# Performance work log

Hardware: AMD Instinct MI355X
Metric: run time of the kernel (lower is better)

## Reference

```python
import jax, jax.numpy as jnp
import numpy as np
from jax import lax

B, N, FIN, T, K, FC, FT = 8, 2048, 3, 12, 3, 64, 64


def _conv2d(x, w, b, pad):
    # x [B,C,N,T], w [O,I,1,kw], NCHW conv
    y = lax.conv_general_dilated(x, w, (1, 1), pad,
                                 dimension_numbers=('NCHW', 'OIHW', 'NCHW'))
    return y + b[None, :, None, None]


def _spatial_att(h, W, a, alpha, concat):
    # GAT-style dense attention. h [B,N,Fin], W [Fin,D], a [2D,1]
    D = W.shape[1]
    Wh = h @ W                                             # [B,N,D]
    e = jax.nn.leaky_relu(Wh @ a[:D] + jnp.swapaxes(Wh @ a[D:], 1, 2), alpha)  # [B,N,N]
    att = jax.nn.softmax(jax.nn.sigmoid(e), axis=1)        # softmax over dim=1 (as in torch)
    hp = jnp.einsum('bij,bjd->bid', att, Wh)
    return jax.nn.elu(hp) if concat else hp


def setup_inputs() -> dict:
    key = jax.random.key(0)
    ks = jax.random.split(key, 24)
    rnd = lambda i, shape, scale=1.0: (jax.random.normal(ks[i], shape, dtype=jnp.float32) * scale)
    FTm = FC * T  # 768 spatial-attention feature dim
    D = FTm // 2
    return {
        'x': rnd(0, (B, N, FIN, T)),
        'cheb': rnd(1, (K, N, N), 1.0 / np.sqrt(N)),
        'Gamma': rnd(2, (K, FIN, FC), 1.0 / np.sqrt(FIN)),
        'W_heads': rnd(3, (2, FTm, D), 1.0 / np.sqrt(FTm)),
        'a_heads': rnd(4, (2, 2 * D, 1), 1.0 / np.sqrt(2 * D)),
        'W_out': rnd(5, (FTm, FTm), 1.0 / np.sqrt(FTm)),
        'a_out': rnd(6, (2 * FTm, 1), 1.0 / np.sqrt(2 * FTm)),
        'U1': rnd(7, (FT, FT), 1.0 / np.sqrt(FT)),
        'U2': rnd(8, (FT,), 1.0 / np.sqrt(FT)),
        'U3': rnd(9, (FT,), 1.0 / np.sqrt(FT)),
        'be': rnd(10, (1, T, T), 0.1),
        'Ve': rnd(11, (T, T), 1.0 / np.sqrt(T)),
        'time_w': rnd(12, (FT, FC, 1, 3), 1.0 / np.sqrt(3 * FC)),
        'time_b': rnd(13, (FT,), 0.01),
        'res_w': rnd(14, (FT, FIN, 1, 1), 1.0 / np.sqrt(FIN)),
        'res_b': rnd(15, (FT,), 0.01),
        'back_w': rnd(16, (FT, FC, 1, 3), 1.0 / np.sqrt(3 * FC)),
        'back_b': rnd(17, (FT,), 0.01),
        'fore_w': rnd(18, (FT, FC, 1, 3), 1.0 / np.sqrt(3 * FC)),
        'fore_b': rnd(19, (FT,), 0.01),
        'ln_g': jnp.ones((FT,), jnp.float32),
        'ln_b': jnp.zeros((FT,), jnp.float32),
    }


def reference(x, cheb, Gamma, W_heads, a_heads, W_out, a_out, U1, U2, U3, be, Ve,
              time_w, time_b, res_w, res_b, back_w, back_b, fore_w, fore_b, ln_g, ln_b):
    b, n, fin, t = x.shape
    k_ = cheb.shape[0]
    fc = Gamma.shape[2]
    # ChebNetII interpolation coefficients T_k(x_j), x_j = cos((j+0.5)pi/K) -> [j,k]
    jj = np.arange(k_)
    cxj = jnp.asarray(np.cos(np.outer((jj + 0.5) * np.pi / k_, np.arange(k_))), x.dtype)
    lhs = jnp.einsum('jio,jk->kio', Gamma, cxj)                         # [K,Fin,Fc]
    rhs = jnp.einsum('bnit,knm->kbmit', x, cheb)                        # [K,B,N,Fin,T]
    spatial_gcn = jax.nn.relu((2.0 / (k_ + 1)) * jnp.einsum('kbmit,kio->bmot', rhs, lhs))  # [B,N,Fc,T]

    # Spatial transformer: 2 GAT heads + output attention
    h = spatial_gcn.reshape(b, n, fc * t)
    heads = jax.vmap(lambda W, a: _spatial_att(h, W, a, 0.1, True))(W_heads, a_heads)  # [H,B,N,D]
    hcat = jnp.transpose(heads, (1, 2, 0, 3)).reshape(b, n, -1)
    gcn_SAt = jax.nn.relu(_spatial_att(hcat, W_out, a_out, 0.1, False)).reshape(b, n, fc, t)

    # Temporal conv (1x3, pad 1)
    tc = _conv2d(jnp.transpose(gcn_SAt, (0, 2, 1, 3)), time_w, time_b, ((0, 0), (1, 1)))
    tc = jnp.transpose(tc, (0, 2, 1, 3))                                # [B,N,Ft,T]

    # Temporal attention
    lhs_t = jnp.einsum('bnft,fg,g->btn', tc, U1, U2)                    # [B,T,N]
    rhs_t = jnp.einsum('f,bnft->bnt', U3, tc)                           # [B,N,T]
    prod = jnp.einsum('bsn,bnt->bst', lhs_t, rhs_t)                     # [B,T,T]
    E = jnp.einsum('is,bst->bit', Ve, jax.nn.sigmoid(prod + be))
    E = jax.nn.softmax(E, axis=1)
    tcn = jnp.einsum('bnft,bts->bnfs', tc, E)                           # [B,N,Ft,T]

    # Residual (1x1 conv) + LayerNorm over channel dim
    x_res = _conv2d(jnp.transpose(x, (0, 2, 1, 3)), res_w, res_b, ((0, 0), (0, 0)))
    x_res = jnp.transpose(x_res, (0, 2, 1, 3))                          # [B,N,Ft,T]
    z = jnp.transpose(jax.nn.relu(x_res + tcn), (0, 3, 1, 2))           # [B,T,N,Ft]
    mu = z.mean(-1, keepdims=True)
    var = z.var(-1, keepdims=True)
    z = (z - mu) / jnp.sqrt(var + 1e-5) * ln_g + ln_b
    result = jnp.transpose(z, (0, 2, 3, 1))                             # [B,N,Ft,T]

    rp = jnp.transpose(result, (0, 2, 1, 3))
    backcast = jnp.transpose(_conv2d(rp, back_w, back_b, ((0, 0), (1, 1))), (0, 2, 1, 3))
    forecast = jnp.transpose(_conv2d(rp, fore_w, fore_b, ((0, 0), (1, 1))), (0, 2, 1, 3))
    return (backcast, forecast)
```

## Files before the change

### kernel.cpp

```cpp
#include <hip/hip_runtime.h>


typedef unsigned short u16;
typedef __bf16 bf16x8 __attribute__((ext_vector_type(8)));
typedef float f32x4 __attribute__((ext_vector_type(4)));
typedef u16 u16x8 __attribute__((ext_vector_type(8)));

__device__ __forceinline__ u16 f2b(float f) {
  union { float f; unsigned u; } v; v.f = f;
  unsigned u = v.u;
  u = u + 0x7FFFu + ((u >> 16) & 1u);
  return (u16)(u >> 16);
}
__device__ __forceinline__ float b2f(u16 h) {
  union { unsigned u; float f; } v; v.u = ((unsigned)h) << 16; return v.f;
}
__device__ __forceinline__ float qfun(float x) {
  float e = x > 0.f ? x : 0.1f * x;
  float s = __builtin_amdgcn_rcpf(1.f + __expf(-e));
  return __expf(s);
}

template <int N> __device__ __forceinline__ void waitvm() {
  if constexpr (N == 0)      asm volatile("s_waitcnt vmcnt(0)" ::: "memory");
  else if constexpr (N == 2) asm volatile("s_waitcnt vmcnt(2)" ::: "memory");
  else if constexpr (N == 4) asm volatile("s_waitcnt vmcnt(4)" ::: "memory");
  else if constexpr (N == 6) asm volatile("s_waitcnt vmcnt(6)" ::: "memory");
  else                       asm volatile("s_waitcnt vmcnt(8)" ::: "memory");
}
__device__ __forceinline__ void rawbar() { asm volatile("s_barrier" ::: "memory"); }

#define GLOAD16(g, l) __builtin_amdgcn_global_load_lds( \
    (__attribute__((address_space(1))) void*)(g),       \
    (__attribute__((address_space(3))) void*)(l), 16, 0, 0)

constexpr size_t OFF_LHS     = 0x0;
constexpr size_t OFF_U1U2    = 0x1000;
constexpr size_t OFF_BIASBIG = 0x1100;
constexpr size_t OFF_FH      = 0x3000;
constexpr size_t OFF_GH      = 0x23000;
constexpr size_t OFF_RDH     = 0x43000;
constexpr size_t OFF_FO      = 0x63000;
constexpr size_t OFF_GO      = 0x73000;
constexpr size_t OFF_RDO     = 0x83000;
constexpr size_t OFF_LHST    = 0x93000;
constexpr size_t OFF_RHST    = 0x153000;
constexpr size_t OFF_PROD    = 0x213000;
constexpr size_t OFF_E       = 0x215000;
constexpr size_t OFF_WCATT   = 0x220000;
constexpr size_t OFF_WOUTT   = 0x340000;
constexpr size_t OFF_WTBIG   = 0x460000;
constexpr size_t OFF_XCOLT   = 0x580000;
constexpr size_t OFF_CHEBT   = 0x700000;
constexpr size_t OFF_C1      = 0x1F00000;
constexpr size_t OFF_H       = 0x4300000;
constexpr size_t OFF_P       = 0x700000;
constexpr size_t OFF_WHCATT  = 0x5B00000;
constexpr size_t OFF_HCAT    = 0x7300000;
constexpr size_t OFF_WHOUTT  = 0x5B00000;
constexpr size_t OFF_GCNB    = 0x7300000;
constexpr size_t OFF_WBFBIG  = 0x8B00000;
constexpr size_t OFF_TCS     = 0x700000;
constexpr size_t OFF_RESULTB = 0x3700000;
constexpr size_t WS_NEEDED   = 0x8D40000;

struct GemmP {
  const u16* A; const u16* BT;
  long sA, sB;
  int K, lda, ldb;
  int swz, splitK;
  float* Cf; long sCf; int ldcf;
  u16* Cb;  long sCb; int ldcb;
  u16* CbT; int ldcT; long sCbT;
  const float* bias;
  float* outB; float* outF;
};

template <int EPI, int WN, int AF = 0>
__global__ __launch_bounds__(256, (WN == 1 ? 3 : 2)) void gemm_bf16(GemmP p) {
  constexpr int BUFU  = AF ? (WN == 1 ? 4096 : 8192) : (WN == 1 ? 8192 : 12288);
  constexpr int SMEMU = 3 * BUFU;
  constexpr int LPWB  = AF ? (WN == 1 ? 2 : 4) : (WN == 1 ? 4 : 6);
  constexpr int WVN   = AF ? (LPWB + 4) : LPWB;
  __shared__ u16 smem[SMEMU];
  const int tid  = threadIdx.x;
  const int lane = tid & 63;
  const int wid  = tid >> 6;
  const int wm = wid >> 1, wn = wid & 1;

  long m0, n0;
  int z = blockIdx.z;
  if (p.swz == 2) {
    int nT = gridDim.x;
    int nwg = nT * gridDim.y;
    long L = (long)blockIdx.z * nwg + blockIdx.x + (long)nT * blockIdx.y;
    z = (int)(L & 7);
    long r = L >> 3;
    m0 = (r / nT) * 128;
    n0 = (r % nT) * (128 * WN);
  } else if (p.swz) {
    int nT = gridDim.x;
    int nwg = nT * gridDim.y;
    int lin = blockIdx.x + nT * blockIdx.y;
    int q = nwg >> 3;
    int swz = (lin & 7) * q + (lin >> 3);
    m0 = (long)(swz / nT) * 128;
    n0 = (long)(swz % nT) * (128 * WN);
  } else {
    m0 = (long)blockIdx.y * 128;
    n0 = (long)blockIdx.x * (128 * WN);
  }

  const int K = p.K;
  long aBase, bBase;
  if (p.splitK) {
    int kz = z >> 2, ch = z & 3;
    aBase = (long)kz * p.sA + (long)ch * 512;
    bBase = (long)ch * 512;
  } else {
    aBase = (long)z * p.sA;
    bBase = (long)z * p.sB;
  }
  const u16* Ab = p.A + aBase + m0 * p.lda;
  const u16* Bb = p.BT + bBase + n0 * p.ldb;

  const int sk = (((lane & 3) ^ ((lane >> 3) & 3))) * 8;
  const u16* aP0 = Ab + (long)(wid * 32 + (lane >> 2)) * p.lda + sk;
  const u16* aP1 = aP0 + (long)16 * p.lda;
  const u16* bP0 = Bb + (long)(wid * 32 * WN + (lane >> 2)) * p.ldb + sk;
  const u16* bP1 = bP0 + (long)16 * p.ldb;
  const u16* bP2 = bP0 + (long)32 * p.ldb;
  const u16* bP3 = bP0 + (long)48 * p.ldb;
  const int aslot = wid * 1024;
  const int bslot = (AF ? 0 : 4096) + wid * (WN == 1 ? 1024 : 2048);

  auto STAGE = [&](int s, int bi) {
    long ko = (long)s * 32;
    u16* base = smem + bi * BUFU;
    if constexpr (!AF) {
      GLOAD16(aP0 + ko, base + aslot);
      GLOAD16(aP1 + ko, base + aslot + 512);
    }
    GLOAD16(bP0 + ko, base + bslot);
    GLOAD16(bP1 + ko, base + bslot + 512);
    if constexpr (WN == 2) {
      GLOAD16(bP2 + ko, base + bslot + 1024);
      GLOAD16(bP3 + ko, base + bslot + 1536);
    }
  };

  f32x4 acc[4][4 * WN];
  f32x4 zero = {0.f, 0.f, 0.f, 0.f};
#pragma unroll
  for (int i = 0; i < 4; ++i)
#pragma unroll
    for (int j = 0; j < 4 * WN; ++j) acc[i][j] = zero;

  const int xorc = (lane >> 1) & 3;
  const int aoff = (wm * 64 + (lane & 15)) * 32 + ((lane >> 4) ^ xorc) * 8;
  const int boff = (AF ? 0 : 4096) + (wn * 64 * WN + (lane & 15)) * 32 + ((lane >> 4) ^ xorc) * 8;

  const int nsteps = K >> 5;
  int cur = 0;

  if constexpr (AF) {
    const long kt512 = (long)(K >> 5) * 512;
    const u16* aPf = p.A + (long)z * p.sA + ((m0 >> 4) + wm * 4) * kt512 + lane * 8;
    bf16x8 avA[4], avB[4];
#pragma unroll
    for (int mi = 0; mi < 4; ++mi) avA[mi] = *(const bf16x8*)(aPf + mi * kt512);
    STAGE(0, 0);
#pragma unroll
    for (int mi = 0; mi < 4; ++mi) avB[mi] = *(const bf16x8*)(aPf + mi * kt512 + 512);
    STAGE(1, 1);
    waitvm<WVN>();
    rawbar();

    auto STEPAF = [&](int i, bf16x8 (&av)[4]) {
      const u16* buf = smem + cur * BUFU;
      bf16x8 bv[4 * WN];
#pragma unroll
      for (int ni = 0; ni < 4 * WN; ++ni) bv[ni] = *(const bf16x8*)&buf[boff + ni * 512];
#pragma unroll
      for (int mi = 0; mi < 4; ++mi)
#pragma unroll
        for (int ni = 0; ni < 4 * WN; ++ni)
          acc[mi][ni] = __builtin_amdgcn_mfma_f32_16x16x32_bf16(av[mi], bv[ni], acc[mi][ni], 0, 0, 0);
      if (i + 1 < nsteps) {
        if (i + 2 < nsteps) {
          STAGE(i + 2, cur == 0 ? 2 : cur - 1);
#pragma unroll
          for (int mi = 0; mi < 4; ++mi)
            av[mi] = *(const bf16x8*)(aPf + mi * kt512 + (long)(i + 2) * 512);
          waitvm<WVN>();
        } else {
          waitvm<0>();
        }
        rawbar();
      }
      cur = (cur == 2) ? 0 : cur + 1;
    };
    for (int i = 0; i < nsteps; i += 2) {
      STEPAF(i, avA);
      if (i + 1 < nsteps) STEPAF(i + 1, avB);
    }
  } else {
    STAGE(0, 0);
    STAGE(1, 1);
    waitvm<WVN>();
    rawbar();
    for (int i = 0; i < nsteps; ++i) {
      const u16* buf = smem + cur * BUFU;
      bf16x8 av[4], bv[4 * WN];
#pragma unroll
      for (int mi = 0; mi < 4; ++mi) av[mi] = *(const bf16x8*)&buf[aoff + mi * 512];
#pragma unroll
      for (int ni = 0; ni < 4 * WN; ++ni) bv[ni] = *(const bf16x8*)&buf[boff + ni * 512];
#pragma unroll
      for (int mi = 0; mi < 4; ++mi)
#pragma unroll
        for (int ni = 0; ni < 4 * WN; ++ni)
          acc[mi][ni] = __builtin_amdgcn_mfma_f32_16x16x32_bf16(av[mi], bv[ni], acc[mi][ni], 0, 0, 0);
      if (i + 1 < nsteps) {
        if (i + 2 < nsteps) {
          STAGE(i + 2, cur == 0 ? 2 : cur - 1);
          waitvm<WVN>();
        } else {
          waitvm<0>();
        }
        rawbar();
      }
      cur = (cur == 2) ? 0 : cur + 1;
    }
  }
  __syncthreads();

  if constexpr (EPI == 1) {
#pragma unroll
    for (int h = 0; h < 2; ++h) {
      if (h == 1) __syncthreads();
      if (WN == 1 || wn == h) {
#pragma unroll
        for (int mi = 0; mi < 4; ++mi)
#pragma unroll
          for (int ni = 0; ni < 4 * WN; ++ni) {
            int cl = (WN == 1 ? wn * 64 : 0) + ni * 16 + (lane & 15);
            int mlb = wm * 64 + mi * 16 + ((lane >> 4) << 2);
#pragma unroll
            for (int r = 0; r < 4; ++r)
              smem[cl * 136 + mlb + r] = f2b(acc[mi][ni][r]);
          }
      }
      __syncthreads();
      int c = tid >> 1, half = tid & 1;
      long bat = m0 >> 11;
      u16* dst = p.CbT + bat * p.sCbT + (long)(n0 + h * 128 + c) * p.ldcT +
                 (m0 & 2047) + half * 64;
      const u16* srcp = &smem[c * 136 + half * 64];
#pragma unroll
      for (int j = 0; j < 64; j += 8)
        *(u16x8*)(dst + j) = *(const u16x8*)(srcp + j);
      if (WN == 1) break;
    }
    return;
  }

  if constexpr (EPI == 7) {
    const int q = lane >> 4, g4 = (lane >> 2) & 3, j = lane & 3;
    const int back = ((int)n0 < 768);
    float* obase = (back ? p.outB : p.outF) - (back ? 0 : 768);
#pragma unroll
    for (int mi = 0; mi < 4; ++mi) {
      long rb0 = m0 + wm * 64 + mi * 16 + q * 4;
#pragma unroll
      for (int ni = 0; ni < 4 * WN; ++ni) {
        int cb = (int)n0 + wn * 64 * WN + ni * 16 + g4 * 4;
        f32x4 v = acc[mi][ni];
        float bsv = p.bias[cb + j];
        v[0] += bsv; v[1] += bsv; v[2] += bsv; v[3] += bsv;
#pragma unroll
        for (int d = 1; d <= 2; d <<= 1) {
          f32x4 t;
#pragma unroll
          for (int b = 0; b < 4; ++b) t[b] = __shfl_xor(v[b ^ d], d, 64);
#pragma unroll
          for (int b = 0; b < 4; ++b) if ((lane ^ b) & d) v[b] = t[b];
        }
        *(f32x4*)(obase + (rb0 + j) * 768 + cb) = v;
      }
    }
    return;
  }

#pragma unroll
  for (int mi = 0; mi < 4; ++mi) {
    long rb0 = m0 + wm * 64 + mi * 16 + ((lane >> 4) << 2);
#pragma unroll
    for (int ni = 0; ni < 4 * WN; ++ni) {
      int col = (int)n0 + wn * 64 * WN + ni * 16 + (lane & 15);
#pragma unroll
      for (int r = 0; r < 4; ++r) {
        float v = acc[mi][ni][r];
        long row = rb0 + r;
        if constexpr (EPI == 2) {
          float e = v > 0.f ? v : expm1f(v);
          p.Cb[(long)z * p.sCb + row * p.ldcb + col] = f2b(e);
        } else if constexpr (EPI == 6) {
          p.Cb[row * 768 + col] = f2b(v + p.bias[col & 63]);
        } else if constexpr (EPI == 9) {
          p.Cb[(long)z * p.sCb + row * p.ldcb + col] = f2b(v);
        } else {
          p.Cb[(long)z * p.sCb + row * p.ldcb + col] = f2b(fmaxf(v, 0.f));
        }
      }
    }
  }
}

__global__ void k_prep(const float* Gamma, const float* U1, const float* U2,
                       const float* back_b, const float* fore_b,
                       float* lhs, float* u1u2, float* biasBig) {
  int o = threadIdx.x;
  if (o < 64) {
    const float cx[3][3] = {{1.f, 0.86602540378443871f, 0.5f},
                            {1.f, 6.123233995736766e-17f, -1.f},
                            {1.f, -0.86602540378443871f, 0.5f}};
    for (int k = 0; k < 3; ++k)
      for (int i = 0; i < 3; ++i) {
        float s = 0;
        for (int j = 0; j < 3; ++j) s += Gamma[(j * 3 + i) * 64 + o] * cx[j][k];
        lhs[(k * 3 + i) * 64 + o] = s;
      }
    float s = 0;
    for (int g = 0; g < 64; ++g) s += U1[o * 64 + g] * U2[g];
    u1u2[o] = s;
    for (int t = 0; t < 12; ++t) {
      biasBig[o * 12 + t] = back_b[o];
      biasBig[768 + o * 12 + t] = fore_b[o];
    }
  }
}

__global__ void k_convert(const float* W_heads, const float* W_out, const float* time_w,
                          const float* back_w, const float* fore_w, const float* xg,
                          u16* WcatT, u16* WoutT, u16* WtBig, u16* WbfBig, u16* xcolT) {
  const int N1 = 589824, NT = 589824, NBF = 1179648, N5 = 786432;
  const int TOT = 2 * N1 + NT + NBF + N5;
  for (int o = blockIdx.x * 256 + threadIdx.x; o < TOT; o += gridDim.x * 256) {
    if (o < N1) {
      int dcol = o / 768, kk = o % 768;
      int hd = dcol / 384, d = dcol % 384;
      WcatT[o] = f2b(W_heads[((long)hd * 768 + kk) * 384 + d]);
    } else if (o < 2 * N1) {
      int o2 = o - N1; int dcol = o2 / 768, kk = o2 % 768;
      WoutT[o2] = f2b(W_out[kk * 768 + dcol]);
    } else if (o < 2 * N1 + NT) {
      int o3 = o - 2 * N1; int col = o3 / 768, kk = o3 % 768;
      int t = col >> 6, ft = col & 63, fc = kk / 12, tau = kk % 12;
      int r = tau - t + 1;
      WtBig[o3] = f2b((r >= 0 && r < 3) ? time_w[ft * 192 + fc * 3 + r] : 0.f);
    } else if (o < 2 * N1 + NT + NBF) {
      int o4 = o - 2 * N1 - NT; int col = o4 / 768, kk = o4 % 768;
      int rem = (col < 768) ? col : col - 768;
      int c = rem / 12, tt = rem % 12;
      int fc = kk / 12, tau = kk % 12; int r = tau - tt + 1;
      const float* wsrc = (col < 768) ? back_w : fore_w;
      WbfBig[o4] = f2b((r >= 0 && r < 3) ? wsrc[c * 192 + fc * 3 + r] : 0.f);
    } else {
      int o5 = o - 2 * N1 - NT - NBF; int c = o5 / 2048, n = o5 % 2048;
      float v = 0.f;
      if (c < 288) {
        int b = c / 36, r2 = c % 36, i = r2 / 12, t = r2 % 12;
        v = xg[(long)(b * 2048 + n) * 36 + i * 12 + t];
      }
      xcolT[o5] = f2b(v);
    }
  }
}

__global__ void k_chebT(const float* cheb, u16* chebT) {
  __shared__ float ts[32][33];
  int n0 = blockIdx.x * 32, m0 = blockIdx.y * 32, k = blockIdx.z;
  int c = threadIdx.x & 31, rq = threadIdx.x >> 5;
  const long base = (long)k * 2048 * 2048;
  for (int q = 0; q < 4; ++q) {
    int n = n0 + rq + q * 8;
    ts[rq + q * 8][c] = cheb[base + (long)n * 2048 + m0 + c];
  }
  __syncthreads();
  for (int q = 0; q < 4; ++q) {
    int m = m0 + rq + q * 8;
    chebT[base + (long)m * 2048 + n0 + c] = f2b(ts[c][rq + q * 8]);
  }
}

__global__ __launch_bounds__(256) void k_h(const u16* C1, const float* lhs, u16* h) {
  int mf = blockIdx.x;
  int tid = threadIdx.x;
  __shared__ float c1s[16][108];
  __shared__ float ls[576];
  __shared__ u16 outb[12288];
  int b = (mf * 16) >> 11;
  for (int s = tid; s < 1728; s += 256) {
    int row = s / 108, rr = s % 108;
    int kk = rr / 12, t = rr % 12; int k = kk / 3, i = kk % 3;
    int n = (mf * 16 + row) & 2047;
    float acc = 0;
#pragma unroll
    for (int ch = 0; ch < 4; ++ch)
      acc += b2f(C1[((long)(k * 4 + ch) * 2048 + n) * 384 + b * 36 + i * 12 + t]);
    c1s[row][rr] = acc;
  }
  for (int s = tid; s < 576; s += 256) ls[s] = lhs[s];
  __syncthreads();
  for (int row = 0; row < 16; ++row) {
#pragma unroll
    for (int j = 0; j < 3; ++j) {
      int e = j * 256 + tid; int o = e / 12, t = e % 12;
      float s = 0;
#pragma unroll
      for (int kk = 0; kk < 9; ++kk) s += c1s[row][kk * 12 + t] * ls[kk * 64 + o];
      s *= 0.5f;
      outb[row * 768 + e] = f2b(s < 0.f ? 0.f : s);
    }
  }
  __syncthreads();
  for (int q = 0; q < 6; ++q) {
    int idx = q * 256 + tid;
    int kt = idx >> 6, lane = idx & 63;
    int m = lane & 15, koct = lane >> 4;
    *(u16x8*)(h + ((long)mf * 24 + kt) * 512 + lane * 8) =
        *(const u16x8*)&outb[m * 768 + kt * 32 + koct * 8];
  }
}

__global__ __launch_bounds__(256) void k_fg(const u16* WhT, int dOff, int Dlen,
                                            const float* aF, const float* aG,
                                            float* fOut, float* gOut) {
  int b = blockIdx.y;
  int i = blockIdx.x * 256 + threadIdx.x;
  __shared__ float af[768], ag[768];
  for (int s = threadIdx.x; s < Dlen; s += 256) { af[s] = aF[s]; ag[s] = aG[s]; }
  __syncthreads();
  const u16* wp = WhT + ((long)b * 768 + dOff) * 2048 + i;
  float fs = 0, gs = 0;
  for (int d = 0; d < Dlen; ++d) {
    float w = b2f(wp[(long)d * 2048]);
    fs += w * af[d]; gs += w * ag[d];
  }
  fOut[b * 2048 + i] = fs;
  gOut[b * 2048 + i] = gs;
}

__global__ __launch_bounds__(256) void k_denom(const float* f, const float* g, float* rd) {
  int b = blockIdx.y;
  int jl = threadIdx.x & 63, ch = threadIdx.x >> 6;
  int j = blockIdx.x * 64 + jl;
  __shared__ float fl[2048];
  __shared__ float red[256];
  for (int s = threadIdx.x; s < 2048; s += 256) fl[s] = f[b * 2048 + s];
  __syncthreads();
  float gj = g[b * 2048 + j];
  float acc = 0;
  for (int i = ch * 512; i < ch * 512 + 512; ++i) acc += qfun(fl[i] + gj);
  red[threadIdx.x] = acc;
  __syncthreads();
  if (ch == 0) {
    float s = red[jl] + red[jl + 64] + red[jl + 128] + red[jl + 192];
    rd[b * 2048 + j] = 1.f / s;
  }
}

__global__ __launch_bounds__(256) void k_Pfrag(const float* f, const float* g,
                                               const float* rd, u16* P) {
  int z = blockIdx.z, mt = blockIdx.y;
  int wid = threadIdx.x >> 6, lane = threadIdx.x & 63;
  int kt = blockIdx.x * 4 + wid;
  const float* fb = f + z * 2048;
  const float* gb = g + z * 2048;
  const float* rb = rd + z * 2048;
  float fv = fb[mt * 16 + (lane & 15)];
  int k0 = kt * 32 + (lane >> 4) * 8;
  float4 g0 = *(const float4*)(gb + k0);
  float4 g1 = *(const float4*)(gb + k0 + 4);
  float4 r0 = *(const float4*)(rb + k0);
  float4 r1 = *(const float4*)(rb + k0 + 4);
  u16x8 o;
  o[0] = f2b(qfun(fv + g0.x) * r0.x);
  o[1] = f2b(qfun(fv + g0.y) * r0.y);
  o[2] = f2b(qfun(fv + g0.z) * r0.z);
  o[3] = f2b(qfun(fv + g0.w) * r0.w);
  o[4] = f2b(qfun(fv + g1.x) * r1.x);
  o[5] = f2b(qfun(fv + g1.y) * r1.y);
  o[6] = f2b(qfun(fv + g1.z) * r1.z);
  o[7] = f2b(qfun(fv + g1.w) * r1.w);
  *(u16x8*)(P + (long)z * 4194304 + ((long)(mt * 64 + kt)) * 512 + lane * 8) = o;
}

__global__ void k_temporal(const u16* tc, const float* u1u2, const float* U3g,
                           float* lhs_t, float* rhs_t) {
  __shared__ float uu[64], u3[64];
  int tid = threadIdx.x;
  if (tid < 64) { uu[tid] = u1u2[tid]; u3[tid] = U3g[tid]; }
  __syncthreads();
  int gid = blockIdx.x * 256 + tid;
  const u16* p = tc + (long)gid * 64;
  float s1 = 0, s2 = 0;
#pragma unroll
  for (int c = 0; c < 8; ++c) {
    u16x8 vv = *(const u16x8*)(p + c * 8);
#pragma unroll
    for (int j = 0; j < 8; ++j) {
      float v = b2f(vv[j]);
      s1 += v * uu[c * 8 + j]; s2 += v * u3[c * 8 + j];
    }
  }
  int t = gid % 12; long bn = gid / 12;
  int b = (int)(bn >> 11);
  lhs_t[((long)b * 12 + t) * 2048 + (int)(bn & 2047)] = s1;
  rhs_t[gid] = s2;
}

__global__ void k_prod(const float* lhs_t, const float* rhs_t, float* prod) {
  int bi = blockIdx.x;
  int b = bi / 144; int r = bi % 144; int s = r / 12; int u = r % 12;
  int tid = threadIdx.x;
  float acc = 0;
  const float* lp = lhs_t + ((long)b * 12 + s) * 2048;
  const float* rp = rhs_t + (long)b * 2048 * 12 + u;
  for (int n = tid; n < 2048; n += 256) acc += lp[n] * rp[n * 12];
  __shared__ float red[256];
  red[tid] = acc; __syncthreads();
  for (int st = 128; st > 0; st >>= 1) {
    if (tid < st) red[tid] += red[tid + st];
    __syncthreads();
  }
  if (tid == 0) prod[bi] = red[0];
}

__global__ void k_E(const float* prod, const float* be, const float* Ve, float* E) {
  int b = blockIdx.x; int tid = threadIdx.x;
  __shared__ float S0[144], E1[144], mx[12], dn[12];
  if (tid < 144) {
    float v = prod[b * 144 + tid] + be[tid];
    S0[tid] = 1.f / (1.f + __expf(-v));
  }
  __syncthreads();
  if (tid < 144) {
    int i = tid / 12, t = tid % 12;
    float a = 0;
    for (int s = 0; s < 12; ++s) a += Ve[i * 12 + s] * S0[s * 12 + t];
    E1[tid] = a;
  }
  __syncthreads();
  if (tid < 12) {
    float m = -1e30f;
    for (int i = 0; i < 12; ++i) m = fmaxf(m, E1[i * 12 + tid]);
    float d = 0;
    for (int i = 0; i < 12; ++i) d += __expf(E1[i * 12 + tid] - m);
    mx[tid] = m; dn[tid] = d;
  }
  __syncthreads();
  if (tid < 144) {
    int t = tid % 12;
    E[b * 144 + tid] = __expf(E1[tid] - mx[t]) / dn[t];
  }
}

__global__ __launch_bounds__(256) void k_res_ln(const u16* tc, const float* E,
                                                const float* xg, const float* res_w,
                                                const float* res_b, const float* ln_g,
                                                const float* ln_b, u16* result) {
  int mf = blockIdx.x; int tid = threadIdx.x;
  int b = (mf * 16) >> 11;
  __shared__ float Eb[144], rw[192], rb[64], lg[64], lb[64];
  __shared__ float tcb[768], zl[768], xl[36], mu[12], rs[12];
  __shared__ u16 outb[12288];
  if (tid < 144) Eb[tid] = E[b * 144 + tid];
  if (tid < 192) rw[tid] = res_w[tid];
  if (tid < 64) { rb[tid] = res_b[tid]; lg[tid] = ln_g[tid]; lb[tid] = ln_b[tid]; }
  for (int r = 0; r < 16; ++r) {
    long bn = (long)mf * 16 + r;
    __syncthreads();
    for (int s = tid; s < 768; s += 256) tcb[s] = b2f(tc[bn * 768 + s]);
    if (tid < 36) xl[tid] = xg[bn * 36 + tid];
    __syncthreads();
    float z[3];
#pragma unroll
    for (int q = 0; q < 3; ++q) {
      int idx = tid + q * 256; int f = idx / 12, s = idx % 12;
      float tcn = 0;
#pragma unroll
      for (int t = 0; t < 12; ++t) tcn += tcb[t * 64 + f] * Eb[t * 12 + s];
      float xr = rb[f];
#pragma unroll
      for (int i = 0; i < 3; ++i) xr += rw[f * 3 + i] * xl[i * 12 + s];
      float v = xr + tcn;
      v = v > 0.f ? v : 0.f;
      z[q] = v; zl[idx] = v;
    }
    __syncthreads();
    if (tid < 12) {
      float m = 0, m2 = 0;
      for (int f = 0; f < 64; ++f) { float v = zl[f * 12 + tid]; m += v; m2 += v * v; }
      m *= (1.f / 64.f); m2 *= (1.f / 64.f);
      mu[tid] = m;
      float var = m2 - m * m;
      rs[tid] = rsqrtf((var > 0.f ? var : 0.f) + 1e-5f);
    }
    __syncthreads();
#pragma unroll
    for (int q = 0; q < 3; ++q) {
      int idx = tid + q * 256; int f = idx / 12, s = idx % 12;
      outb[r * 768 + idx] = f2b((z[q] - mu[s]) * rs[s] * lg[f] + lb[f]);
    }
  }
  __syncthreads();
  for (int q = 0; q < 6; ++q) {
    int idx = q * 256 + tid;
    int kt = idx >> 6, lane = idx & 63;
    int m = lane & 15, koct = lane >> 4;
    *(u16x8*)(result + ((long)mf * 24 + kt) * 512 + lane * 8) =
        *(const u16x8*)&outb[m * 768 + kt * 32 + koct * 8];
  }
}

__global__ void k_sentinel(float* out, long n) {
  long i = (long)blockIdx.x * 256 + threadIdx.x;
  if (i < n) out[i] = 12345.0f;
}

extern "C" void kernel_launch(void* const* d_in, const int* in_sizes, int n_in,
                              void* d_out, int out_size, void* d_ws, size_t ws_size,
                              hipStream_t stream) {
  (void)in_sizes; (void)n_in;
  const float* x       = (const float*)d_in[0];
  const float* cheb    = (const float*)d_in[1];
  const float* Gamma   = (const float*)d_in[2];
  const float* W_heads = (const float*)d_in[3];
  const float* a_heads = (const float*)d_in[4];
  const float* W_out   = (const float*)d_in[5];
  const float* a_out   = (const float*)d_in[6];
  const float* U1      = (const float*)d_in[7];
  const float* U2      = (const float*)d_in[8];
  const float* U3      = (const float*)d_in[9];
  const float* be      = (const float*)d_in[10];
  const float* Ve      = (const float*)d_in[11];
  const float* time_w  = (const float*)d_in[12];
  const float* time_b  = (const float*)d_in[13];
  const float* res_w   = (const float*)d_in[14];
  const float* res_b   = (const float*)d_in[15];
  const float* back_w  = (const float*)d_in[16];
  const float* back_b  = (const float*)d_in[17];
  const float* fore_w  = (const float*)d_in[18];
  const float* fore_b  = (const float*)d_in[19];
  const float* ln_g    = (const float*)d_in[20];
  const float* ln_b    = (const float*)d_in[21];
  float* out = (float*)d_out;

  if (ws_size < WS_NEEDED) {
    k_sentinel<<<(out_size + 255) / 256, 256, 0, stream>>>(out, out_size);
    return;
  }

  char* ws = (char*)d_ws;
  float* lhs     = (float*)(ws + OFF_LHS);
  float* u1u2    = (float*)(ws + OFF_U1U2);
  float* biasBig = (float*)(ws + OFF_BIASBIG);
  float* fH      = (float*)(ws + OFF_FH);
  float* gH      = (float*)(ws + OFF_GH);
  float* rdH     = (float*)(ws + OFF_RDH);
  float* fO      = (float*)(ws + OFF_FO);
  float* gO      = (float*)(ws + OFF_GO);
  float* rdO     = (float*)(ws + OFF_RDO);
  float* lhs_t   = (float*)(ws + OFF_LHST);
  float* rhs_t   = (float*)(ws + OFF_RHST);
  float* prod    = (float*)(ws + OFF_PROD);
  float* Ebuf    = (float*)(ws + OFF_E);
  u16* WcatT   = (u16*)(ws + OFF_WCATT);
  u16* WoutT   = (u16*)(ws + OFF_WOUTT);
  u16* WtBig   = (u16*)(ws + OFF_WTBIG);
  u16* WbfBig  = (u16*)(ws + OFF_WBFBIG);
  u16* xcolT   = (u16*)(ws + OFF_XCOLT);
  u16* chebT   = (u16*)(ws + OFF_CHEBT);
  u16* C1      = (u16*)(ws + OFF_C1);
  u16* hbuf    = (u16*)(ws + OFF_H);
  u16* Pbuf    = (u16*)(ws + OFF_P);
  u16* WhcatT  = (u16*)(ws + OFF_WHCATT);
  u16* hcat    = (u16*)(ws + OFF_HCAT);
  u16* WhoutT  = (u16*)(ws + OFF_WHOUTT);
  u16* gcnB    = (u16*)(ws + OFF_GCNB);
  u16* tcsB    = (u16*)(ws + OFF_TCS);
  u16* resultB = (u16*)(ws + OFF_RESULTB);

  k_prep<<<1, 64, 0, stream>>>(Gamma, U1, U2, back_b, fore_b, lhs, u1u2, biasBig);
  k_convert<<<2048, 256, 0, stream>>>(W_heads, W_out, time_w, back_w, fore_w, x,
                                      WcatT, WoutT, WtBig, WbfBig, xcolT);
  k_chebT<<<dim3(64, 64, 3), 256, 0, stream>>>(cheb, chebT);

  {
    GemmP p{}; p.A = chebT; p.BT = xcolT; p.sA = 2048L * 2048; p.sB = 0;
    p.K = 512; p.lda = 2048; p.ldb = 2048; p.splitK = 1; p.swz = 1;
    p.Cb = C1; p.sCb = 2048L * 384; p.ldcb = 384;
    gemm_bf16<9, 1><<<dim3(3, 16, 12), 256, 0, stream>>>(p);
  }
  k_h<<<1024, 256, 0, stream>>>(C1, lhs, hbuf);

  {
    GemmP p{}; p.A = hbuf; p.BT = WcatT; p.sA = 0; p.sB = 0;
    p.K = 768; p.lda = 768; p.ldb = 768; p.swz = 1;
    p.CbT = WhcatT; p.ldcT = 2048; p.sCbT = 768L * 2048;
    gemm_bf16<1, 2, 1><<<dim3(3, 128, 1), 256, 0, stream>>>(p);
  }
  k_fg<<<dim3(8, 8), 256, 0, stream>>>(WhcatT, 0, 384, a_heads, a_heads + 384, fH, gH);
  k_fg<<<dim3(8, 8), 256, 0, stream>>>(WhcatT, 384, 384, a_heads + 768, a_heads + 1152,
                                       fH + 16384, gH + 16384);
  for (int hd = 0; hd < 2; ++hd) {
    const float* f = fH + hd * 16384; const float* g = gH + hd * 16384;
    float* rd = rdH + hd * 16384;
    k_denom<<<dim3(32, 8), 256, 0, stream>>>(f, g, rd);
    k_Pfrag<<<dim3(16, 128, 8), 256, 0, stream>>>(f, g, rd, Pbuf);
    GemmP p{}; p.A = Pbuf; p.BT = WhcatT + (long)hd * 384 * 2048;
    p.sA = 2048L * 2048; p.sB = 768L * 2048;
    p.K = 2048; p.lda = 2048; p.ldb = 2048; p.swz = 2;
    p.Cb = hcat + hd * 384; p.sCb = 2048L * 768; p.ldcb = 768;
    gemm_bf16<2, 1, 1><<<dim3(3, 16, 8), 256, 0, stream>>>(p);
  }

  {
    GemmP p{}; p.A = hcat; p.BT = WoutT; p.sA = 0; p.sB = 0;
    p.K = 768; p.lda = 768; p.ldb = 768; p.swz = 1;
    p.CbT = WhoutT; p.ldcT = 2048; p.sCbT = 768L * 2048;
    gemm_bf16<1, 2><<<dim3(3, 128, 1), 256, 0, stream>>>(p);
  }
  k_fg<<<dim3(8, 8), 256, 0, stream>>>(WhoutT, 0, 768, a_out, a_out + 768, fO, gO);
  k_denom<<<dim3(32, 8), 256, 0, stream>>>(fO, gO, rdO);
  k_Pfrag<<<dim3(16, 128, 8), 256, 0, stream>>>(fO, gO, rdO, Pbuf);
  {
    GemmP p{}; p.A = Pbuf; p.BT = WhoutT; p.sA = 2048L * 2048; p.sB = 768L * 2048;
    p.K = 2048; p.lda = 2048; p.ldb = 2048; p.swz = 2;
    p.Cb = gcnB; p.sCb = 2048L * 768; p.ldcb = 768;
    gemm_bf16<8, 2, 1><<<dim3(3, 16, 8), 256, 0, stream>>>(p);
  }

  {
    GemmP p{}; p.A = gcnB; p.BT = WtBig; p.sA = 0; p.sB = 0;
    p.K = 768; p.lda = 768; p.ldb = 768; p.swz = 1;
    p.Cb = tcsB; p.bias = time_b;
    gemm_bf16<6, 2><<<dim3(3, 128, 1), 256, 0, stream>>>(p);
  }

  k_temporal<<<768, 256, 0, stream>>>(tcsB, u1u2, U3, lhs_t, rhs_t);
  k_prod<<<1152, 256, 0, stream>>>(lhs_t, rhs_t, prod);
  k_E<<<8, 256, 0, stream>>>(prod, be, Ve, Ebuf);

  k_res_ln<<<1024, 256, 0, stream>>>(tcsB, Ebuf, x, res_w, res_b, ln_g, ln_b, resultB);

  {
    GemmP p{}; p.A = resultB; p.BT = WbfBig; p.sA = 0; p.sB = 0;
    p.K = 768; p.lda = 768; p.ldb = 768; p.swz = 1;
    p.bias = biasBig; p.outB = out; p.outF = out + 12582912L;
    gemm_bf16<7, 2, 1><<<dim3(6, 128, 1), 256, 0, stream>>>(p);
  }
}
```

Measured before the change: 722.2 us.

## Add LDS-free fragment-layout GEMM for head projection and backcast/forecast

Adds a new GEMM kernel that loads A and B straight from global memory into registers in MFMA fragment order, with three register stages in flight and no LDS staging. The weight-conversion kernel now writes WcatT and WbfBig pre-packed in 16x32 fragment tiles so these loads are contiguous per lane. The two 768-K GEMMs (Wh projection and the final backcast/forecast conv) switch to this kernel with 128x128 tiles and a grouped tile swizzle, doubling the grid in N. The aim is to remove LDS round-trips and barriers. The cost is more register pressure and no cross-wave reuse of loaded tiles through shared memory.

```diff
diff --git a/kernel.cpp b/kernel.cpp
--- a/kernel.cpp
+++ b/kernel.cpp
@@ -22,11 +22,12 @@
 }
 
 template <int N> __device__ __forceinline__ void waitvm() {
-  if constexpr (N == 0)      asm volatile("s_waitcnt vmcnt(0)" ::: "memory");
-  else if constexpr (N == 2) asm volatile("s_waitcnt vmcnt(2)" ::: "memory");
-  else if constexpr (N == 4) asm volatile("s_waitcnt vmcnt(4)" ::: "memory");
-  else if constexpr (N == 6) asm volatile("s_waitcnt vmcnt(6)" ::: "memory");
-  else                       asm volatile("s_waitcnt vmcnt(8)" ::: "memory");
+  if constexpr (N == 0)       asm volatile("s_waitcnt vmcnt(0)" ::: "memory");
+  else if constexpr (N == 2)  asm volatile("s_waitcnt vmcnt(2)" ::: "memory");
+  else if constexpr (N == 4)  asm volatile("s_waitcnt vmcnt(4)" ::: "memory");
+  else if constexpr (N == 6)  asm volatile("s_waitcnt vmcnt(6)" ::: "memory");
+  else if constexpr (N == 8)  asm volatile("s_waitcnt vmcnt(8)" ::: "memory");
+  else                        asm volatile("s_waitcnt vmcnt(16)" ::: "memory");
 }
 __device__ __forceinline__ void rawbar() { asm volatile("s_barrier" ::: "memory"); }
 
@@ -76,6 +77,114 @@
   float* outB; float* outF;
 };
 
+template <int EPI>
+__global__ __launch_bounds__(256, 2) void gemm_afb(GemmP p) {
+  __shared__ u16 smem[(EPI == 1) ? 17408 : 16];
+  const int tid = threadIdx.x, lane = tid & 63, wid = tid >> 6;
+  const int wm = wid >> 1, wn = wid & 1;
+  const int z = blockIdx.z;
+  int nT = gridDim.x;
+  int nwg = nT * gridDim.y;
+  int lin = blockIdx.x + nT * blockIdx.y;
+  int q8 = nwg >> 3;
+  int sw = (lin & 7) * q8 + (lin >> 3);
+  long m0 = (long)(sw / nT) * 128;
+  long n0 = (long)(sw % nT) * 128;
+
+  const int KT = p.K >> 5;
+  const long mstr = (long)KT * 512;
+  const u16* aPf = p.A + (long)z * p.sA + ((m0 >> 4) + wm * 4) * mstr + lane * 8;
+  const u16* bPf = p.BT + ((n0 >> 4) + wn * 4) * mstr + lane * 8;
+
+  f32x4 acc[4][4];
+  f32x4 zero = {0.f, 0.f, 0.f, 0.f};
+#pragma unroll
+  for (int i = 0; i < 4; ++i)
+#pragma unroll
+    for (int j = 0; j < 4; ++j) acc[i][j] = zero;
+
+  bf16x8 a0[4], b0[4], a1[4], b1[4], a2[4], b2[4];
+  auto LOAD = [&](bf16x8 (&av)[4], bf16x8 (&bv)[4], int s) {
+#pragma unroll
+    for (int mi = 0; mi < 4; ++mi) av[mi] = *(const bf16x8*)(aPf + mi * mstr + (long)s * 512);
+#pragma unroll
+    for (int ni = 0; ni < 4; ++ni) bv[ni] = *(const bf16x8*)(bPf + ni * mstr + (long)s * 512);
+  };
+  auto MM = [&](bf16x8 (&av)[4], bf16x8 (&bv)[4]) {
+#pragma unroll
+    for (int mi = 0; mi < 4; ++mi)
+#pragma unroll
+      for (int ni = 0; ni < 4; ++ni)
+        acc[mi][ni] = __builtin_amdgcn_mfma_f32_16x16x32_bf16(av[mi], bv[ni], acc[mi][ni], 0, 0, 0);
+  };
+
+  LOAD(a0, b0, 0);
+  if (KT > 1) LOAD(a1, b1, 1);
+  if (KT > 2) LOAD(a2, b2, 2);
+  for (int i = 0; i < KT; i += 3) {
+    waitvm<16>(); MM(a0, b0);
+    if (i + 3 < KT) LOAD(a0, b0, i + 3);
+    if (i + 1 < KT) {
+      waitvm<16>(); MM(a1, b1);
+      if (i + 4 < KT) LOAD(a1, b1, i + 4);
+    }
+    if (i + 2 < KT) {
+      waitvm<16>(); MM(a2, b2);
+      if (i + 5 < KT) LOAD(a2, b2, i + 5);
+    }
+  }
+
+  if constexpr (EPI == 1) {
+    __syncthreads();
+#pragma unroll
+    for (int mi = 0; mi < 4; ++mi)
+#pragma unroll
+      for (int ni = 0; ni < 4; ++ni) {
+        int cl = wn * 64 + ni * 16 + (lane & 15);
+        int mlb = wm * 64 + mi * 16 + ((lane >> 4) << 2);
+#pragma unroll
+        for (int r = 0; r < 4; ++r)
+          smem[cl * 136 + mlb + r] = f2b(acc[mi][ni][r]);
+      }
+    __syncthreads();
+    int c = tid >> 1, half = tid & 1;
+    long bat = m0 >> 11;
+    u16* dst = p.CbT + bat * p.sCbT + (long)(n0 + c) * p.ldcT + (m0 & 2047) + half * 64;
+    const u16* srcp = &smem[c * 136 + half * 64];
+#pragma unroll
+    for (int j = 0; j < 64; j += 8)
+      *(u16x8*)(dst + j) = *(const u16x8*)(srcp + j);
+    return;
+  }
+
+  if constexpr (EPI == 7) {
+    const int q = lane >> 4, g4 = (lane >> 2) & 3, j = lane & 3;
+    const int back = ((int)n0 < 768);
+    float* obase = (back ? p.outB : p.outF) - (back ? 0 : 768);
+#pragma unroll
+    for (int mi = 0; mi < 4; ++mi) {
+      long rb0 = m0 + wm * 64 + mi * 16 + q * 4;
+#pragma unroll
+      for (int ni = 0; ni < 4; ++ni) {
+        int cb = (int)n0 + wn * 64 + ni * 16 + g4 * 4;
+        f32x4 v = acc[mi][ni];
+        float bsv = p.bias[cb + j];
+        v[0] += bsv; v[1] += bsv; v[2] += bsv; v[3] += bsv;
+#pragma unroll
+        for (int d = 1; d <= 2; d <<= 1) {
+          f32x4 t;
+#pragma unroll
+          for (int b = 0; b < 4; ++b) t[b] = __shfl_xor(v[b ^ d], d, 64);
+#pragma unroll
+          for (int b = 0; b < 4; ++b) if ((lane ^ b) & d) v[b] = t[b];
+        }
+        *(f32x4*)(obase + (rb0 + j) * 768 + cb) = v;
+      }
+    }
+    return;
+  }
+}
+
 template <int EPI, int WN, int AF = 0>
 __global__ __launch_bounds__(256, (WN == 1 ? 3 : 2)) void gemm_bf16(GemmP p) {
   constexpr int BUFU  = AF ? (WN == 1 ? 4096 : 8192) : (WN == 1 ? 8192 : 12288);
@@ -265,33 +374,6 @@
     return;
   }
 
-  if constexpr (EPI == 7) {
-    const int q = lane >> 4, g4 = (lane >> 2) & 3, j = lane & 3;
-    const int back = ((int)n0 < 768);
-    float* obase = (back ? p.outB : p.outF) - (back ? 0 : 768);
-#pragma unroll
-    for (int mi = 0; mi < 4; ++mi) {
-      long rb0 = m0 + wm * 64 + mi * 16 + q * 4;
-#pragma unroll
-      for (int ni = 0; ni < 4 * WN; ++ni) {
-        int cb = (int)n0 + wn * 64 * WN + ni * 16 + g4 * 4;
-        f32x4 v = acc[mi][ni];
-        float bsv = p.bias[cb + j];
-        v[0] += bsv; v[1] += bsv; v[2] += bsv; v[3] += bsv;
-#pragma unroll
-        for (int d = 1; d <= 2; d <<= 1) {
-          f32x4 t;
-#pragma unroll
-          for (int b = 0; b < 4; ++b) t[b] = __shfl_xor(v[b ^ d], d, 64);
-#pragma unroll
-          for (int b = 0; b < 4; ++b) if ((lane ^ b) & d) v[b] = t[b];
-        }
-        *(f32x4*)(obase + (rb0 + j) * 768 + cb) = v;
-      }
-    }
-    return;
-  }
-
 #pragma unroll
   for (int mi = 0; mi < 4; ++mi) {
     long rb0 = m0 + wm * 64 + mi * 16 + ((lane >> 4) << 2);
@@ -348,7 +430,11 @@
   const int TOT = 2 * N1 + NT + NBF + N5;
   for (int o = blockIdx.x * 256 + threadIdx.x; o < TOT; o += gridDim.x * 256) {
     if (o < N1) {
-      int dcol = o / 768, kk = o % 768;
+      int f = o >> 9, s = o & 511;
+      int ln = s >> 3, j = s & 7;
+      int nf = f / 24, kt = f % 24;
+      int dcol = nf * 16 + (ln & 15);
+      int kk = kt * 32 + (ln >> 4) * 8 + j;
       int hd = dcol / 384, d = dcol % 384;
       WcatT[o] = f2b(W_heads[((long)hd * 768 + kk) * 384 + d]);
     } else if (o < 2 * N1) {
@@ -360,7 +446,12 @@
       int r = tau - t + 1;
       WtBig[o3] = f2b((r >= 0 && r < 3) ? time_w[ft * 192 + fc * 3 + r] : 0.f);
     } else if (o < 2 * N1 + NT + NBF) {
-      int o4 = o - 2 * N1 - NT; int col = o4 / 768, kk = o4 % 768;
+      int o4 = o - 2 * N1 - NT;
+      int f = o4 >> 9, s = o4 & 511;
+      int ln = s >> 3, j = s & 7;
+      int nf = f / 24, kt = f % 24;
+      int col = nf * 16 + (ln & 15);
+      int kk = kt * 32 + (ln >> 4) * 8 + j;
       int rem = (col < 768) ? col : col - 768;
       int c = rem / 12, tt = rem % 12;
       int fc = kk / 12, tau = kk % 12; int r = tau - tt + 1;
@@ -707,10 +798,9 @@
   k_h<<<1024, 256, 0, stream>>>(C1, lhs, hbuf);
 
   {
-    GemmP p{}; p.A = hbuf; p.BT = WcatT; p.sA = 0; p.sB = 0;
-    p.K = 768; p.lda = 768; p.ldb = 768; p.swz = 1;
+    GemmP p{}; p.A = hbuf; p.BT = WcatT; p.sA = 0; p.K = 768;
     p.CbT = WhcatT; p.ldcT = 2048; p.sCbT = 768L * 2048;
-    gemm_bf16<1, 2, 1><<<dim3(3, 128, 1), 256, 0, stream>>>(p);
+    gemm_afb<1><<<dim3(6, 128, 1), 256, 0, stream>>>(p);
   }
   k_fg<<<dim3(8, 8), 256, 0, stream>>>(WhcatT, 0, 384, a_heads, a_heads + 384, fH, gH);
   k_fg<<<dim3(8, 8), 256, 0, stream>>>(WhcatT, 384, 384, a_heads + 768, a_heads + 1152,
@@ -757,9 +847,8 @@
   k_res_ln<<<1024, 256, 0, stream>>>(tcsB, Ebuf, x, res_w, res_b, ln_g, ln_b, resultB);
 
   {
-    GemmP p{}; p.A = resultB; p.BT = WbfBig; p.sA = 0; p.sB = 0;
-    p.K = 768; p.lda = 768; p.ldb = 768; p.swz = 1;
+    GemmP p{}; p.A = resultB; p.BT = WbfBig; p.sA = 0; p.K = 768;
     p.bias = biasBig; p.outB = out; p.outF = out + 12582912L;
-    gemm_bf16<7, 2, 1><<<dim3(6, 128, 1), 256, 0, stream>>>(p);
-  }
-}
+    gemm_afb<7><<<dim3(12, 128, 1), 256, 0, stream>>>(p);
+  }
+}
```

Result: no change. 717.7 us (-0.6%).
